# Kernel tuning notes

Measured on AMD Instinct MI355X. Metric: run time of the kernel, lower is better.

Reference implementation:

```python
import jax, jax.numpy as jnp
import numpy as np

E, H, I = 16, 2048, 768
B, S = 4, 1024
TOPK = 8
BLK_R, BLK_C = 128, 128


def blockwise_dequantize(w, scale_inv, r, c):
    # w: [E, M, N] (fp8 values stored as fp32 here), scale_inv: [E, M//r, N//c]
    e, m, n = w.shape
    wb = w.reshape(e, m // r, r, n // c, c)
    wb = wb * scale_inv[:, :, None, :, None]
    return wb.reshape(e, m, n)


def setup_inputs() -> dict:
    key = jax.random.key(0)
    ks = jax.random.split(key, 7)
    return {
        "hidden_states": jax.random.normal(ks[0], (B, S, H), dtype=jnp.float32),
        "routing_weights": jax.random.uniform(ks[1], (B * S, E), dtype=jnp.float32),
        "gate_up_proj": jax.random.normal(ks[2], (E, H, 2 * I), dtype=jnp.float32),
        "gate_up_proj_scale_inv": jax.random.uniform(ks[3], (E, H // BLK_R, 2 * I // BLK_C), dtype=jnp.float32),
        "down_proj": jax.random.normal(ks[4], (E, I, H), dtype=jnp.float32),
        "down_proj_scale_inv": jax.random.uniform(ks[5], (E, I // BLK_R, H // BLK_C), dtype=jnp.float32),
        "router_indices": jax.random.randint(ks[6], (B * S, TOPK), 0, E, dtype=jnp.int64 if jax.config.jax_enable_x64 else jnp.int32),
    }


def reference(hidden_states, routing_weights, gate_up_proj, gate_up_proj_scale_inv,
              down_proj, down_proj_scale_inv, router_indices):
    batch_size = hidden_states.shape[0]
    hs = hidden_states.reshape(-1, H)                      # [T, H], T = B*S
    x = jnp.broadcast_to(hs[None], (E,) + hs.shape)        # repeat across experts

    gu_w = blockwise_dequantize(gate_up_proj, gate_up_proj_scale_inv, BLK_R, BLK_C)   # [E, H, 2I]
    dn_w = blockwise_dequantize(down_proj, down_proj_scale_inv, BLK_R, BLK_C)         # [E, I, H]

    gate_up = jnp.einsum('eth,ehf->etf', x, gu_w)          # [E, T, 2I]
    gate, up = jnp.split(gate_up, 2, axis=-1)
    inter = up * jax.nn.silu(gate)                         # [E, T, I]
    next_states = jnp.einsum('eti,eih->eth', inter, dn_w)  # [E, T, H]

    next_states = next_states.reshape(E, batch_size, -1, H)
    rw = routing_weights.T.reshape(E, batch_size, -1)      # [E, B, S]
    out = (next_states * rw[..., None]).sum(axis=0)        # [B, S, H]
    return out
```

## Files before the change

### kernel.cpp

```cpp
#include <hip/hip_runtime.h>
#include <hip/hip_bf16.h>
#include <cstdint>

#define E_     16
#define H_     2048
#define I_     768
#define T_     4096
#define TWO_I  1536
#define K2_    (E_ * I_)

typedef __bf16 bf16x8 __attribute__((ext_vector_type(8)));
typedef float  floatx4 __attribute__((ext_vector_type(4)));

__device__ __forceinline__ void gload_lds16(const void* g, void* l) {
  __builtin_amdgcn_global_load_lds(
      (const __attribute__((address_space(1))) void*)(void*)g,
      (__attribute__((address_space(3))) void*)l,
      16, 0, 0);
}

#define ASM_VMCNT(n) asm volatile("s_waitcnt vmcnt(" #n ")" ::: "memory")
#define ASM_LGKM(n)  asm volatile("s_waitcnt lgkmcnt(" #n ")" ::: "memory")
#define SBAR()       __builtin_amdgcn_s_barrier()
#define SCHED0()     __builtin_amdgcn_sched_barrier(0)
#define PRIO1()      __builtin_amdgcn_s_setprio(1)
#define PRIO0()      __builtin_amdgcn_s_setprio(0)

__device__ __forceinline__ void dq_body(const float* __restrict__ src,
                                        __bf16* __restrict__ dst,
                                        const float* __restrict__ scale,
                                        int e, int n0, int m0, int R, int C,
                                        size_t slab, size_t rowStride, int ilvHalf,
                                        float* tile) {
  const float s = scale[((size_t)e * (R >> 7) + (m0 >> 7)) * (C >> 7) + (n0 >> 7)];
  const float* sp = src + ((size_t)e * R + m0) * C + n0;
  const int t  = threadIdx.x;
  const int c4 = (t & 15) * 4;
  const int rb = t >> 4;
  #pragma unroll
  for (int p = 0; p < 4; ++p) {
    int r = p * 16 + rb;
    float4 v = *(const float4*)(sp + (size_t)r * C + c4);
    tile[(c4 + 0) * 65 + r] = v.x * s;
    tile[(c4 + 1) * 65 + r] = v.y * s;
    tile[(c4 + 2) * 65 + r] = v.z * s;
    tile[(c4 + 3) * 65 + r] = v.w * s;
  }
  __syncthreads();
  const int c8 = (t & 7) * 8;
  const int r0 = t >> 3;
  #pragma unroll
  for (int p = 0; p < 2; ++p) {
    int nr = r0 + p * 32;
    int ng = n0 + nr;
    int np;
    if (ilvHalf) {
      int h = (ng >= ilvHalf) ? 1 : 0;
      int iLoc = ng - h * ilvHalf;
      np = ((iLoc >> 5) << 6) + h * 32 + (iLoc & 31);
    } else {
      np = ng;
    }
    const float* row = &tile[nr * 65 + c8];
    bf16x8 o;
    #pragma unroll
    for (int j = 0; j < 8; ++j) o[j] = (__bf16)row[j];
    *(bf16x8*)(dst + (size_t)e * slab + (size_t)np * rowStride + m0 + c8) = o;
  }
}

__global__ void k_prep(const float* __restrict__ hs, __bf16* __restrict__ hsb,
                       const float* __restrict__ gup, __bf16* __restrict__ wgu,
                       const float* __restrict__ gups,
                       const float* __restrict__ dnp, __bf16* __restrict__ wdn,
                       const float* __restrict__ dnps) {
  __shared__ float tile[64 * 65];
  const int id = blockIdx.x;
  if (id < 4096) {
    size_t idx = ((size_t)id * blockDim.x + threadIdx.x) * 8;
    float4 a = *(const float4*)(hs + idx);
    float4 b = *(const float4*)(hs + idx + 4);
    bf16x8 o;
    o[0] = (__bf16)a.x; o[1] = (__bf16)a.y; o[2] = (__bf16)a.z; o[3] = (__bf16)a.w;
    o[4] = (__bf16)b.x; o[5] = (__bf16)b.y; o[6] = (__bf16)b.z; o[7] = (__bf16)b.w;
    *(bf16x8*)(hsb + idx) = o;
  } else if (id < 4096 + 12288) {
    const int id2 = id - 4096;
    const int bx = id2 % 24;
    const int rest = id2 / 24;
    const int by = rest & 31;
    const int e  = rest >> 5;
    dq_body(gup, wgu, gups, e, bx * 64, by * 64, H_, TWO_I,
            (size_t)TWO_I * H_, (size_t)H_, I_, tile);
  } else {
    const int id3 = id - (4096 + 12288);
    const int bx = id3 & 31;
    const int rest = id3 >> 5;
    const int by = rest % 12;
    const int e  = rest / 12;
    dq_body(dnp, wdn, dnps, e, bx * 64, by * 64, I_, H_,
            (size_t)I_, (size_t)K2_, 0, tile);
  }
}

#define STG_A(tt, h) do { int b_ = ((tt)&1)*16384 + (h)*8192; \
    gload_lds16(aSrc + (size_t)((h)*128)*LDK + (tt)*64, dA + b_); \
    gload_lds16(aSrc + (size_t)((h)*128 + 64)*LDK + (tt)*64, dA + b_ + 4096); } while (0)
#define STG_B(tt, h) do { int b_ = ((tt)&1)*16384 + (h)*8192; \
    gload_lds16(bSrc + (size_t)((h)*128)*LDK + (tt)*64, dB + b_); \
    gload_lds16(bSrc + (size_t)((h)*128 + 64)*LDK + (tt)*64, dB + b_ + 4096); } while (0)

#define AFLD(DST, MI0) do { \
    DST[0][0] = *(const bf16x8*)(pA + (MI0)*1024 + kc0); \
    DST[0][1] = *(const bf16x8*)(pA + (MI0)*1024 + kc1); \
    DST[1][0] = *(const bf16x8*)(pA + ((MI0)+1)*1024 + kc0); \
    DST[1][1] = *(const bf16x8*)(pA + ((MI0)+1)*1024 + kc1); } while (0)

#define BBLD() do { \
    _Pragma("unroll") \
    for (int ni = 0; ni < 4; ++ni) { \
      bb[ni][0] = *(const bf16x8*)(pB + ni * 1024 + kc0); \
      bb[ni][1] = *(const bf16x8*)(pB + ni * 1024 + kc1); \
    } } while (0)

#define MFMA16(MI0, AF) do { \
    _Pragma("unroll") \
    for (int ii = 0; ii < 2; ++ii) { \
      _Pragma("unroll") \
      for (int ni = 0; ni < 4; ++ni) { \
        acc[(MI0)+ii][ni] = __builtin_amdgcn_mfma_f32_16x16x32_bf16(AF[ii][0], bb[ni][0], acc[(MI0)+ii][ni], 0, 0, 0); \
        acc[(MI0)+ii][ni] = __builtin_amdgcn_mfma_f32_16x16x32_bf16(AF[ii][1], bb[ni][1], acc[(MI0)+ii][ni], 0, 0, 0); \
      } \
    } } while (0)

#define TILE_BODY_STAGED(tt, NT) do { \
    const int bo = ((tt) & 1) * 16384; \
    const __bf16* pA = pArd + bo; \
    const __bf16* pB = pBrd + bo; \
    bf16x8 bb[4][2], afA[2][2], afB[2][2]; \
    BBLD(); \
    AFLD(afA, 0); \
     \
    AFLD(afB, 2); \
    STG_A((tt) + 1, 0); \
    SBAR(); ASM_LGKM(4); SCHED0(); \
    PRIO1(); MFMA16(0, afA); PRIO0(); SBAR(); \
     \
    AFLD(afA, 4); \
    STG_A((tt) + 1, 1); \
    SBAR(); ASM_LGKM(4); SCHED0(); \
    PRIO1(); MFMA16(2, afB); PRIO0(); SBAR(); \
     \
    AFLD(afB, 6); \
    if ((tt) + 2 < (NT)) STG_B((tt) + 2, 0); \
    SBAR(); ASM_LGKM(4); SCHED0(); \
    PRIO1(); MFMA16(4, afA); PRIO0(); SBAR(); \
     \
    if ((tt) + 2 < (NT)) { STG_B((tt) + 2, 1); ASM_VMCNT(4); } \
    else                 { ASM_VMCNT(0); } \
    SBAR(); ASM_LGKM(0); SCHED0(); \
    PRIO1(); MFMA16(6, afB); PRIO0(); SBAR(); \
  } while (0)

#define TILE_BODY_LAST(tt) do { \
    const int bo = ((tt) & 1) * 16384; \
    const __bf16* pA = pArd + bo; \
    const __bf16* pB = pBrd + bo; \
    bf16x8 bb[4][2], afA[2][2], afB[2][2]; \
    BBLD(); \
    AFLD(afA, 0); \
    AFLD(afB, 2); \
    SBAR(); ASM_LGKM(4); SCHED0(); \
    PRIO1(); MFMA16(0, afA); PRIO0(); SBAR(); \
    AFLD(afA, 4); \
    SBAR(); ASM_LGKM(4); SCHED0(); \
    PRIO1(); MFMA16(2, afB); PRIO0(); SBAR(); \
    AFLD(afB, 6); \
    SBAR(); ASM_LGKM(4); SCHED0(); \
    PRIO1(); MFMA16(4, afA); PRIO0(); SBAR(); \
    SBAR(); ASM_LGKM(0); SCHED0(); \
    PRIO1(); MFMA16(6, afB); PRIO0(); SBAR(); \
  } while (0)

__global__ __launch_bounds__(512, 2)
void k_gemm1(const __bf16* __restrict__ A, const __bf16* __restrict__ W,
             const float* __restrict__ rw, __bf16* __restrict__ inter) {
  extern __shared__ __align__(16) __bf16 smem[];
  __bf16* sA = smem;
  __bf16* sB = smem + 32768;
  float*  sRW = (float*)(smem + 65536);

  const int lid = blockIdx.x + 16 * (blockIdx.y + 6 * blockIdx.z);
  const int nid = (lid & 7) * 192 + (lid >> 3);
  const int e  = nid / 96;
  const int r_ = nid - e * 96;
  const int by = r_ >> 4;
  const int m0 = (r_ & 15) * 256;
  const int n0 = by * 256;

  const int t    = threadIdx.x;
  const int wave = t >> 6, lane = t & 63;
  const int wm = wave >> 2, wn = wave & 3;
  const int l4 = lane >> 4, r16 = lane & 15;
  const int LDK = H_;

  if (t < 256) sRW[t] = rw[(size_t)(m0 + t) * E_ + e];

  const int rowSt = t >> 3;
  const int kcSt  = ((t & 7) ^ ((t >> 3) & 7)) << 3;
  const __bf16* aSrc = A + (size_t)(m0 + rowSt) * H_ + kcSt;
  const __bf16* bSrc = W + ((size_t)e * TWO_I + n0 + rowSt) * H_ + kcSt;
  __bf16* dA = sA + wave * 512;
  __bf16* dB = sB + wave * 512;

  const int kc0 = (l4 ^ (r16 & 7)) << 3;
  const int kc1 = ((4 + l4) ^ (r16 & 7)) << 3;
  const __bf16* pArd = sA + wm * 8192 + r16 * 64;
  const __bf16* pBrd = sB + (wn >> 1) * 8192 + ((wn & 1) * 64 + r16) * 64;

  floatx4 acc[8][4];
  #pragma unroll
  for (int mi = 0; mi < 8; ++mi)
    #pragma unroll
    for (int ni = 0; ni < 4; ++ni) {
      floatx4 z = {0.f, 0.f, 0.f, 0.f};
      acc[mi][ni] = z;
    }

  STG_B(0, 0); STG_B(0, 1); STG_A(0, 0); STG_A(0, 1);
  STG_B(1, 0); STG_B(1, 1);
  ASM_VMCNT(0);
  SBAR();

  const int NT = H_ / 64;
  for (int tt = 0; tt < NT - 1; ++tt) {
    TILE_BODY_STAGED(tt, NT);
  }
  TILE_BODY_LAST(NT - 1);

  const int rq = l4 * 4;
  const int gBase = (by * 4 + wn) * 32;
  #pragma unroll
  for (int mi = 0; mi < 8; ++mi) {
    const int rl = wm * 128 + mi * 16 + rq;
    #pragma unroll
    for (int ni = 0; ni < 2; ++ni) {
      const size_t colIdx = (size_t)e * I_ + gBase + ni * 16 + r16;
      #pragma unroll
      for (int r = 0; r < 4; ++r) {
        float g = acc[mi][ni][r];
        float u = acc[mi][ni + 2][r];
        float sil = g / (1.0f + __expf(-g));
        float val = u * sil * sRW[rl + r];
        inter[(size_t)(m0 + rl + r) * K2_ + colIdx] = (__bf16)val;
      }
    }
  }
}

__global__ __launch_bounds__(512, 2)
void k_gemm2(const __bf16* __restrict__ Ainter, const __bf16* __restrict__ W,
             float* __restrict__ out0, float* __restrict__ out1) {
  extern __shared__ __align__(16) __bf16 smem[];
  __bf16* sA = smem;
  __bf16* sB = smem + 32768;

  const int lid = blockIdx.x + 16 * (blockIdx.y + 8 * blockIdx.z);
  const int nid = (lid & 7) * 32 + (lid >> 3);
  const int bz = nid >> 7;
  const int r_ = nid & 127;
  const int n0 = (r_ >> 4) * 256;
  const int m0 = (r_ & 15) * 256;
  float* dst = bz ? out1 : out0;
  const size_t kOff = (size_t)bz * (K2_ / 2);

  const int t    = threadIdx.x;
  const int wave = t >> 6, lane = t & 63;
  const int wm = wave >> 2, wn = wave & 3;
  const int l4 = lane >> 4, r16 = lane & 15;
  const int LDK = K2_;

  const int rowSt = t >> 3;
  const int kcSt  = ((t & 7) ^ ((t >> 3) & 7)) << 3;
  const __bf16* aSrc = Ainter + (size_t)(m0 + rowSt) * K2_ + kOff + kcSt;
  const __bf16* bSrc = W      + (size_t)(n0 + rowSt) * K2_ + kOff + kcSt;
  __bf16* dA = sA + wave * 512;
  __bf16* dB = sB + wave * 512;

  const int kc0 = (l4 ^ (r16 & 7)) << 3;
  const int kc1 = ((4 + l4) ^ (r16 & 7)) << 3;
  const __bf16* pArd = sA + wm * 8192 + r16 * 64;
  const __bf16* pBrd = sB + (wn >> 1) * 8192 + ((wn & 1) * 64 + r16) * 64;

  floatx4 acc[8][4];
  #pragma unroll
  for (int mi = 0; mi < 8; ++mi)
    #pragma unroll
    for (int ni = 0; ni < 4; ++ni) {
      floatx4 z = {0.f, 0.f, 0.f, 0.f};
      acc[mi][ni] = z;
    }

  STG_B(0, 0); STG_B(0, 1); STG_A(0, 0); STG_A(0, 1);
  STG_B(1, 0); STG_B(1, 1);
  ASM_VMCNT(0);
  SBAR();

  const int NT = (K2_ / 2) / 64;
  for (int tt = 0; tt < NT - 1; ++tt) {
    TILE_BODY_STAGED(tt, NT);
  }
  TILE_BODY_LAST(NT - 1);

  const int rq = l4 * 4;
  #pragma unroll
  for (int mi = 0; mi < 8; ++mi) {
    const int rl = wm * 128 + mi * 16 + rq;
    #pragma unroll
    for (int ni = 0; ni < 4; ++ni) {
      const int cl = wn * 64 + ni * 16 + r16;
      #pragma unroll
      for (int r = 0; r < 4; ++r)
        dst[(size_t)(m0 + rl + r) * H_ + n0 + cl] = acc[mi][ni][r];
    }
  }
}

__global__ void k_addout(float* __restrict__ out, const float* __restrict__ part) {
  size_t i = ((size_t)blockIdx.x * blockDim.x + threadIdx.x) * 4;
  float4 a = *(const float4*)(out + i);
  float4 b = *(const float4*)(part + i);
  a.x += b.x; a.y += b.y; a.z += b.z; a.w += b.w;
  *(float4*)(out + i) = a;
}

extern "C" void kernel_launch(void* const* d_in, const int* in_sizes, int n_in,
                              void* d_out, int out_size, void* d_ws, size_t ws_size,
                              hipStream_t stream) {
  const float* hs   = (const float*)d_in[0];
  const float* rw   = (const float*)d_in[1];
  const float* gup  = (const float*)d_in[2];
  const float* gups = (const float*)d_in[3];
  const float* dnp  = (const float*)d_in[4];
  const float* dnps = (const float*)d_in[5];
  float* out = (float*)d_out;

  char* ws = (char*)d_ws;
  __bf16* hsb  = (__bf16*)ws;
  __bf16* wgu  = (__bf16*)(ws + (size_t)(16 << 20));
  __bf16* wdn  = (__bf16*)(ws + (size_t)(112 << 20));
  __bf16* intr = (__bf16*)(ws + (size_t)(160 << 20));
  float* part = (float*)(ws + (size_t)(16 << 20));

  static int inited = 0;
  if (!inited) {
    hipFuncSetAttribute((const void*)k_gemm1,
                        hipFuncAttributeMaxDynamicSharedMemorySize, 132096);
    hipFuncSetAttribute((const void*)k_gemm2,
                        hipFuncAttributeMaxDynamicSharedMemorySize, 131072);
    inited = 1;
  }

  k_prep<<<4096 + 12288 + 6144, 256, 0, stream>>>(hs, hsb, gup, wgu, gups,
                                                  dnp, wdn, dnps);
  k_gemm1<<<dim3(T_ / 256, TWO_I / 256, E_), 512, 132096, stream>>>(hsb, wgu, rw, intr);
  k_gemm2<<<dim3(T_ / 256, H_ / 256, 2), 512, 131072, stream>>>(intr, wdn, out, part);
  k_addout<<<(T_ * H_) / (256 * 4), 256, 0, stream>>>(out, part);
}
```

Before: 918.7 us.

## Simplify GEMM tile pipeline to single A-fragment buffer and split gemm1 launch

```diff
diff --git a/kernel.cpp b/kernel.cpp
--- a/kernel.cpp
+++ b/kernel.cpp
@@ -20,7 +20,7 @@
 }
 
 #define ASM_VMCNT(n) asm volatile("s_waitcnt vmcnt(" #n ")" ::: "memory")
-#define ASM_LGKM(n)  asm volatile("s_waitcnt lgkmcnt(" #n ")" ::: "memory")
+#define ASM_LGKM0()  asm volatile("s_waitcnt lgkmcnt(0)" ::: "memory")
 #define SBAR()       __builtin_amdgcn_s_barrier()
 #define SCHED0()     __builtin_amdgcn_sched_barrier(0)
 #define PRIO1()      __builtin_amdgcn_s_setprio(1)
@@ -110,11 +110,11 @@
     gload_lds16(bSrc + (size_t)((h)*128)*LDK + (tt)*64, dB + b_); \
     gload_lds16(bSrc + (size_t)((h)*128 + 64)*LDK + (tt)*64, dB + b_ + 4096); } while (0)
 
-#define AFLD(DST, MI0) do { \
-    DST[0][0] = *(const bf16x8*)(pA + (MI0)*1024 + kc0); \
-    DST[0][1] = *(const bf16x8*)(pA + (MI0)*1024 + kc1); \
-    DST[1][0] = *(const bf16x8*)(pA + ((MI0)+1)*1024 + kc0); \
-    DST[1][1] = *(const bf16x8*)(pA + ((MI0)+1)*1024 + kc1); } while (0)
+#define AF4(MI0) do { \
+    af[0][0] = *(const bf16x8*)(pA + (MI0)*1024 + kc0); \
+    af[0][1] = *(const bf16x8*)(pA + (MI0)*1024 + kc1); \
+    af[1][0] = *(const bf16x8*)(pA + ((MI0)+1)*1024 + kc0); \
+    af[1][1] = *(const bf16x8*)(pA + ((MI0)+1)*1024 + kc1); } while (0)
 
 #define BBLD() do { \
     _Pragma("unroll") \
@@ -123,77 +123,55 @@
       bb[ni][1] = *(const bf16x8*)(pB + ni * 1024 + kc1); \
     } } while (0)
 
-#define MFMA16(MI0, AF) do { \
+#define MFMA16(MI0) do { \
     _Pragma("unroll") \
     for (int ii = 0; ii < 2; ++ii) { \
       _Pragma("unroll") \
       for (int ni = 0; ni < 4; ++ni) { \
-        acc[(MI0)+ii][ni] = __builtin_amdgcn_mfma_f32_16x16x32_bf16(AF[ii][0], bb[ni][0], acc[(MI0)+ii][ni], 0, 0, 0); \
-        acc[(MI0)+ii][ni] = __builtin_amdgcn_mfma_f32_16x16x32_bf16(AF[ii][1], bb[ni][1], acc[(MI0)+ii][ni], 0, 0, 0); \
+        acc[(MI0)+ii][ni] = __builtin_amdgcn_mfma_f32_16x16x32_bf16(af[ii][0], bb[ni][0], acc[(MI0)+ii][ni], 0, 0, 0); \
+        acc[(MI0)+ii][ni] = __builtin_amdgcn_mfma_f32_16x16x32_bf16(af[ii][1], bb[ni][1], acc[(MI0)+ii][ni], 0, 0, 0); \
       } \
     } } while (0)
 
-#define TILE_BODY_STAGED(tt, NT) do { \
+#define PHASE(MI0, STAGE_STMT, CKPT_STMT) do { \
+    AF4(MI0); \
+    STAGE_STMT; \
+    CKPT_STMT; \
+    SBAR(); \
+    ASM_LGKM0(); \
+    SCHED0(); \
+    PRIO1(); \
+    MFMA16(MI0); \
+    PRIO0(); \
+    SBAR(); \
+  } while (0)
+
+#define TILE_BODY(tt, NT) do { \
     const int bo = ((tt) & 1) * 16384; \
     const __bf16* pA = pArd + bo; \
     const __bf16* pB = pBrd + bo; \
-    bf16x8 bb[4][2], afA[2][2], afB[2][2]; \
+    bf16x8 bb[4][2], af[2][2]; \
     BBLD(); \
-    AFLD(afA, 0); \
-     \
-    AFLD(afB, 2); \
-    STG_A((tt) + 1, 0); \
-    SBAR(); ASM_LGKM(4); SCHED0(); \
-    PRIO1(); MFMA16(0, afA); PRIO0(); SBAR(); \
-     \
-    AFLD(afA, 4); \
-    STG_A((tt) + 1, 1); \
-    SBAR(); ASM_LGKM(4); SCHED0(); \
-    PRIO1(); MFMA16(2, afB); PRIO0(); SBAR(); \
-     \
-    AFLD(afB, 6); \
-    if ((tt) + 2 < (NT)) STG_B((tt) + 2, 0); \
-    SBAR(); ASM_LGKM(4); SCHED0(); \
-    PRIO1(); MFMA16(4, afA); PRIO0(); SBAR(); \
-     \
-    if ((tt) + 2 < (NT)) { STG_B((tt) + 2, 1); ASM_VMCNT(4); } \
-    else                 { ASM_VMCNT(0); } \
-    SBAR(); ASM_LGKM(0); SCHED0(); \
-    PRIO1(); MFMA16(6, afB); PRIO0(); SBAR(); \
-  } while (0)
-
-#define TILE_BODY_LAST(tt) do { \
-    const int bo = ((tt) & 1) * 16384; \
-    const __bf16* pA = pArd + bo; \
-    const __bf16* pB = pBrd + bo; \
-    bf16x8 bb[4][2], afA[2][2], afB[2][2]; \
-    BBLD(); \
-    AFLD(afA, 0); \
-    AFLD(afB, 2); \
-    SBAR(); ASM_LGKM(4); SCHED0(); \
-    PRIO1(); MFMA16(0, afA); PRIO0(); SBAR(); \
-    AFLD(afA, 4); \
-    SBAR(); ASM_LGKM(4); SCHED0(); \
-    PRIO1(); MFMA16(2, afB); PRIO0(); SBAR(); \
-    AFLD(afB, 6); \
-    SBAR(); ASM_LGKM(4); SCHED0(); \
-    PRIO1(); MFMA16(4, afA); PRIO0(); SBAR(); \
-    SBAR(); ASM_LGKM(0); SCHED0(); \
-    PRIO1(); MFMA16(6, afB); PRIO0(); SBAR(); \
+    PHASE(0, if ((tt) + 1 < (NT)) STG_A((tt) + 1, 0), (void)0); \
+    PHASE(2, if ((tt) + 1 < (NT)) STG_A((tt) + 1, 1), (void)0); \
+    PHASE(4, if ((tt) + 2 < (NT)) STG_B((tt) + 2, 0), (void)0); \
+    PHASE(6, if ((tt) + 2 < (NT)) STG_B((tt) + 2, 1), \
+             if ((tt) + 2 < (NT)) { ASM_VMCNT(4); } else { ASM_VMCNT(0); }); \
   } while (0)
 
 __global__ __launch_bounds__(512, 2)
 void k_gemm1(const __bf16* __restrict__ A, const __bf16* __restrict__ W,
-             const float* __restrict__ rw, __bf16* __restrict__ inter) {
+             const float* __restrict__ rw, __bf16* __restrict__ inter,
+             int eOff) {
   extern __shared__ __align__(16) __bf16 smem[];
   __bf16* sA = smem;
   __bf16* sB = smem + 32768;
   float*  sRW = (float*)(smem + 65536);
 
   const int lid = blockIdx.x + 16 * (blockIdx.y + 6 * blockIdx.z);
-  const int nid = (lid & 7) * 192 + (lid >> 3);
-  const int e  = nid / 96;
-  const int r_ = nid - e * 96;
+  const int nid = (lid & 7) * 96 + (lid >> 3);
+  const int e  = eOff + nid / 96;
+  const int r_ = nid % 96;
   const int by = r_ >> 4;
   const int m0 = (r_ & 15) * 256;
   const int n0 = by * 256;
@@ -233,10 +211,9 @@
   SBAR();
 
   const int NT = H_ / 64;
-  for (int tt = 0; tt < NT - 1; ++tt) {
-    TILE_BODY_STAGED(tt, NT);
-  }
-  TILE_BODY_LAST(NT - 1);
+  for (int tt = 0; tt < NT; ++tt) {
+    TILE_BODY(tt, NT);
+  }
 
   const int rq = l4 * 4;
   const int gBase = (by * 4 + wn) * 32;
@@ -307,10 +284,9 @@
   SBAR();
 
   const int NT = (K2_ / 2) / 64;
-  for (int tt = 0; tt < NT - 1; ++tt) {
-    TILE_BODY_STAGED(tt, NT);
-  }
-  TILE_BODY_LAST(NT - 1);
+  for (int tt = 0; tt < NT; ++tt) {
+    TILE_BODY(tt, NT);
+  }
 
   const int rq = l4 * 4;
   #pragma unroll
@@ -363,7 +339,8 @@
 
   k_prep<<<4096 + 12288 + 6144, 256, 0, stream>>>(hs, hsb, gup, wgu, gups,
                                                   dnp, wdn, dnps);
-  k_gemm1<<<dim3(T_ / 256, TWO_I / 256, E_), 512, 132096, stream>>>(hsb, wgu, rw, intr);
+  k_gemm1<<<dim3(16, 6, 8), 512, 132096, stream>>>(hsb, wgu, rw, intr, 0);
+  k_gemm1<<<dim3(16, 6, 8), 512, 132096, stream>>>(hsb, wgu, rw, intr, 8);
   k_gemm2<<<dim3(T_ / 256, H_ / 256, 2), 512, 131072, stream>>>(intr, wdn, out, part);
   k_addout<<<(T_ * H_) / (256 * 4), 256, 0, stream>>>(out, part);
 }
```

Measured after the change: 905.0 us. About the same (-1.5%).
